# Optimization experiments

Measured on AMD Instinct MI355X. Metric: run time of the kernel, lower is better.

Reference implementation:

```python
import jax, jax.numpy as jnp
import numpy as np

ALPHA = 0.2  # leaky relu slope
NEG_BIG = -9e15


def setup_inputs() -> dict:
    key = jax.random.key(0)
    k1, k2, k3, k4 = jax.random.split(key, 4)
    B, N, Fin, Fout = 8, 2048, 128, 128
    h = jax.random.normal(k1, (B, N, Fin), dtype=jnp.float32)
    adj = jax.random.randint(k2, (N, N), 0, 2, dtype=jnp.int32)
    # xavier_uniform with gain=1.414
    limW = 1.414 * np.sqrt(6.0 / (Fin + Fout))
    W = jax.random.uniform(k3, (Fin, Fout), minval=-limW, maxval=limW, dtype=jnp.float32)
    lima = 1.414 * np.sqrt(6.0 / (2 * Fout + 1))
    a = jax.random.uniform(k4, (2 * Fout, 1), minval=-lima, maxval=lima, dtype=jnp.float32)
    return {"h": h, "adj": adj, "W": W, "a": a}


def reference(h, adj, W, a):
    # Wh: [B, N, F]
    Wh = jnp.einsum("bnf,fo->bno", h, W)
    Fout = W.shape[1]
    a1, a2 = a[:Fout, 0], a[Fout:, 0]  # [F], [F]
    # Additive score decomposition (same math as concat trick):
    # e[b,i,j] = leakyrelu(Wh_i . a1 + Wh_j . a2)
    s1 = Wh @ a1  # [B, N] (source/query part)
    s2 = Wh @ a2  # [B, N] (target part)
    e = s1[:, :, None] + s2[:, None, :]  # [B, N, N]
    e = jnp.where(e > 0, e, ALPHA * e)   # leaky relu
    e = jnp.where(adj[None, :, :] > 0, e, NEG_BIG)
    attention = jax.nn.softmax(e, axis=2)  # [B, N, N]
    # dropout is identity in eval mode
    h_prime = jnp.einsum("bij,bjf->bif", attention, Wh)
    return h_prime
```

## Files before the change

### kernel.cpp

```cpp
#include <hip/hip_runtime.h>
#include <hip/hip_bf16.h>
#include <stdint.h>

#define ALPHA 0.2f

typedef __attribute__((ext_vector_type(8))) short bf16x8;
typedef __attribute__((ext_vector_type(4))) float f32x4;

__device__ __forceinline__ short f2bf(float f) {
    union { float f; uint32_t u; } c; c.f = f;
    uint32_t u = c.u + 0x7FFF + ((c.u >> 16) & 1);
    return (short)(u >> 16);
}

__global__ __launch_bounds__(256) void pack_adj_kernel(
        const int* __restrict__ adj, uint8_t* __restrict__ bytes,
        const float* __restrict__ W, short* __restrict__ WTg) {
    int t = blockIdx.x * 256 + threadIdx.x;
    const int4* a4 = reinterpret_cast<const int4*>(adj) + (size_t)t * 2;
    int4 x0 = a4[0], x1 = a4[1];
    uint32_t m = 0;
    m |= (x0.x > 0) ? 1u   : 0u;  m |= (x0.y > 0) ? 2u   : 0u;
    m |= (x0.z > 0) ? 4u   : 0u;  m |= (x0.w > 0) ? 8u   : 0u;
    m |= (x1.x > 0) ? 16u  : 0u;  m |= (x1.y > 0) ? 32u  : 0u;
    m |= (x1.z > 0) ? 64u  : 0u;  m |= (x1.w > 0) ? 128u : 0u;
    bytes[t] = (uint8_t)m;

    if (blockIdx.x < 64) {
        int idx = blockIdx.x * 256 + threadIdx.x;
        int k = idx >> 7, f = idx & 127;
        WTg[f * 128 + k] = f2bf(W[k * 128 + f]);
    }
}

__global__ __launch_bounds__(256) void wh_kernel(
        const float* __restrict__ h, const short* __restrict__ WTg,
        const float* __restrict__ a, short* __restrict__ whT,
        float* __restrict__ s1g, float* __restrict__ s2g) {
    __shared__ float sred[4][2][16];
    __shared__ short tr[4][32][24];

    int tid = threadIdx.x, wid = tid >> 6, lane = tid & 63;
    int q = lane >> 4, n = lane & 15;
    int rb = blockIdx.x * 16;
    int row = rb + n;

    f32x4 acc[2] = {};
    #pragma unroll
    for (int kc = 0; kc < 4; ++kc) {
        const float* hp = h + (size_t)row * 128 + kc * 32 + q * 8;
        float4 h0 = reinterpret_cast<const float4*>(hp)[0];
        float4 h1 = reinterpret_cast<const float4*>(hp)[1];
        bf16x8 afrag;
        afrag[0] = f2bf(h0.x); afrag[1] = f2bf(h0.y);
        afrag[2] = f2bf(h0.z); afrag[3] = f2bf(h0.w);
        afrag[4] = f2bf(h1.x); afrag[5] = f2bf(h1.y);
        afrag[6] = f2bf(h1.z); afrag[7] = f2bf(h1.w);
        #pragma unroll
        for (int u = 0; u < 2; ++u) {
            int t = wid * 2 + u;
            bf16x8 bfrag = *reinterpret_cast<const bf16x8*>(
                WTg + (t * 16 + n) * 128 + kc * 32 + q * 8);
            acc[u] = __builtin_amdgcn_mfma_f32_16x16x32_bf16(afrag, bfrag, acc[u], 0, 0, 0);
        }
    }

    float p1[4] = {0.f, 0.f, 0.f, 0.f}, p2[4] = {0.f, 0.f, 0.f, 0.f};
    #pragma unroll
    for (int u = 0; u < 2; ++u) {
        int c = (wid * 2 + u) * 16 + n;
        float a1c = a[c], a2c = a[128 + c];
        #pragma unroll
        for (int r = 0; r < 4; ++r) {
            p1[r] += acc[u][r] * a1c;
            p2[r] += acc[u][r] * a2c;
        }
    }
    #pragma unroll
    for (int d = 1; d < 16; d <<= 1) {
        #pragma unroll
        for (int r = 0; r < 4; ++r) {
            p1[r] += __shfl_xor(p1[r], d);
            p2[r] += __shfl_xor(p2[r], d);
        }
    }
    if (n == 0) {
        #pragma unroll
        for (int r = 0; r < 4; ++r) {
            sred[wid][0][q * 4 + r] = p1[r];
            sred[wid][1][q * 4 + r] = p2[r];
        }
    }

    #pragma unroll
    for (int u = 0; u < 2; ++u)
        #pragma unroll
        for (int r = 0; r < 4; ++r)
            tr[wid][u * 16 + n][q * 4 + r] = f2bf(acc[u][r]);
    __syncthreads();

    if (wid == 0 && lane < 16) {
        float v1 = 0.f, v2 = 0.f;
        #pragma unroll
        for (int v = 0; v < 4; ++v) { v1 += sred[v][0][lane]; v2 += sred[v][1][lane]; }
        s1g[rb + lane] = v1;
        s2g[rb + lane] = v2;
    }

    int bb = rb >> 11, jr = rb & 2047;
    int fl = lane & 31, jh = lane >> 5;
    bf16x8 v = *reinterpret_cast<const bf16x8*>(&tr[wid][fl][jh * 8]);
    int f = wid * 32 + fl;
    *reinterpret_cast<bf16x8*>(whT + ((size_t)(bb * 128 + f) * 2048) + jr + jh * 8) = v;
}

__global__ __launch_bounds__(512) void attn_kernel(
        const short* __restrict__ whT, const float* __restrict__ s1g,
        const float* __restrict__ s2g, const uint8_t* __restrict__ adjb,
        float* __restrict__ out) {
    __shared__ f32x4 buf[8][8][64];
    __shared__ float lds_ds[8][2][16];

    int wid = threadIdx.x >> 6, lane = threadIdx.x & 63;
    int q = lane >> 4, n = lane & 15;
    int b  = blockIdx.x >> 6;
    int ib = (blockIdx.x & 63) * 32;
    int rowA = ib + n, rowB = ib + 16 + n;

    float s1A = s1g[b * 2048 + rowA];
    float s1B = s1g[b * 2048 + rowB];
    const float*   s2b  = s2g + b * 2048;
    const short*   whTb = whT + (size_t)b * 262144;
    const uint8_t* adjA = adjb + (size_t)rowA * 256;
    const uint8_t* adjB = adjb + (size_t)rowB * 256;

    f32x4 accA[8] = {}, accB[8] = {};
    float dsA = 0.f, dsB = 0.f;
    int jbase = wid * 256;

    for (int c = 0; c < 8; ++c) {
        int k0 = jbase + c * 32 + q * 8;
        uint32_t mA = adjA[k0 >> 3];
        uint32_t mB = adjB[k0 >> 3];
        float4 s2a = *reinterpret_cast<const float4*>(s2b + k0);
        float4 s2c = *reinterpret_cast<const float4*>(s2b + k0 + 4);
        float s2arr[8] = {s2a.x, s2a.y, s2a.z, s2a.w, s2c.x, s2c.y, s2c.z, s2c.w};

        bf16x8 afA, afB;
        #pragma unroll
        for (int j = 0; j < 8; ++j) {
            float eA = s1A + s2arr[j];
            eA = fmaxf(eA, ALPHA * eA);
            float pA = ((mA >> j) & 1) ? __expf(eA) : 0.0f;
            dsA += pA; afA[j] = f2bf(pA);
            float eB = s1B + s2arr[j];
            eB = fmaxf(eB, ALPHA * eB);
            float pB = ((mB >> j) & 1) ? __expf(eB) : 0.0f;
            dsB += pB; afB[j] = f2bf(pB);
        }

        const short* bp = whTb + k0;
        #pragma unroll
        for (int t = 0; t < 8; ++t) {
            bf16x8 bf = *reinterpret_cast<const bf16x8*>(bp + (size_t)(t * 16 + n) * 2048);
            accA[t] = __builtin_amdgcn_mfma_f32_16x16x32_bf16(afA, bf, accA[t], 0, 0, 0);
            accB[t] = __builtin_amdgcn_mfma_f32_16x16x32_bf16(afB, bf, accB[t], 0, 0, 0);
        }
    }

    dsA += __shfl_xor(dsA, 16); dsA += __shfl_xor(dsA, 32);
    dsB += __shfl_xor(dsB, 16); dsB += __shfl_xor(dsB, 32);
    if (q == 0) { lds_ds[wid][0][n] = dsA; lds_ds[wid][1][n] = dsB; }

    #pragma unroll
    for (int i = 0; i < 8; ++i) buf[wid][i][lane] = accA[i];
    __syncthreads();

    f32x4 sA = buf[0][wid][lane];
    #pragma unroll
    for (int v = 1; v < 8; ++v) sA += buf[v][wid][lane];

    float dAt = 0.f, dBt = 0.f;
    #pragma unroll
    for (int v = 0; v < 8; ++v) { dAt += lds_ds[v][0][n]; dBt += lds_ds[v][1][n]; }
    float rdA[4], rdB[4];
    #pragma unroll
    for (int r = 0; r < 4; ++r) {
        rdA[r] = 1.0f / __shfl(dAt, q * 4 + r);
        rdB[r] = 1.0f / __shfl(dBt, q * 4 + r);
    }

    size_t ob = ((size_t)b * 2048 + ib) * 128;
    #pragma unroll
    for (int r = 0; r < 4; ++r)
        out[ob + (size_t)(q * 4 + r) * 128 + wid * 16 + n] = sA[r] * rdA[r];
    __syncthreads();

    #pragma unroll
    for (int i = 0; i < 8; ++i) buf[wid][i][lane] = accB[i];
    __syncthreads();

    f32x4 sB = buf[0][wid][lane];
    #pragma unroll
    for (int v = 1; v < 8; ++v) sB += buf[v][wid][lane];
    #pragma unroll
    for (int r = 0; r < 4; ++r)
        out[ob + (size_t)(16 + q * 4 + r) * 128 + wid * 16 + n] = sB[r] * rdB[r];
}

extern "C" void kernel_launch(void* const* d_in, const int* in_sizes, int n_in,
                              void* d_out, int out_size, void* d_ws, size_t ws_size,
                              hipStream_t stream) {
    const float* h   = (const float*)d_in[0];
    const int*   adj = (const int*)d_in[1];
    const float* W   = (const float*)d_in[2];
    const float* a   = (const float*)d_in[3];
    float* out = (float*)d_out;

    char* ws = (char*)d_ws;
    short* whT = (short*)ws;
    float* s1  = (float*)(ws + 4194304);
    float* s2  = (float*)(ws + 4259840);
    uint8_t* bytes = (uint8_t*)(ws + 4325376);

    short* WTg = (short*)d_out + (4194304 - 16384);

    pack_adj_kernel<<<2048, 256, 0, stream>>>(adj, bytes, W, WTg);
    wh_kernel<<<1024, 256, 0, stream>>>(h, WTg, a, whT, s1, s2);
    attn_kernel<<<512, 512, 0, stream>>>(whT, s1, s2, bytes, out);
}
```

Measured before the change: 127.1 us.

## Software-pipeline attention loads, halve waves per block, pack bf16 with perm

The attention kernel now runs 4 waves per block instead of 8, so each wave handles 512 columns over 16 fully unrolled steps. It double-buffers the next step's whT fragments, adjacency mask words and s2 values in registers while the current step computes. Mask reads move from bytes to 32-bit words, and the float-to-bf16 conversion uses a perm-based pack with simpler rounding. The cross-wave reduction is reshaped so each wave sums two output tiles from four partials. The aim is to hide global load latency behind exp and MFMA work, at the cost of higher register pressure under a 3-blocks-per-SM launch bound and fewer waves per block.

```diff
diff --git a/kernel.cpp b/kernel.cpp
--- a/kernel.cpp
+++ b/kernel.cpp
@@ -11,6 +11,12 @@
     union { float f; uint32_t u; } c; c.f = f;
     uint32_t u = c.u + 0x7FFF + ((c.u >> 16) & 1);
     return (short)(u >> 16);
+}
+
+__device__ __forceinline__ uint32_t pk_bf16(float lo, float hi) {
+    union { float f; uint32_t u; } a, b;
+    a.f = lo; b.f = hi;
+    return __builtin_amdgcn_perm(b.u + 0x8000u, a.u + 0x8000u, 0x07060302u);
 }
 
 __global__ __launch_bounds__(256) void pack_adj_kernel(
@@ -114,57 +120,86 @@
     *reinterpret_cast<bf16x8*>(whT + ((size_t)(bb * 128 + f) * 2048) + jr + jh * 8) = v;
 }
 
-__global__ __launch_bounds__(512) void attn_kernel(
+__global__ __launch_bounds__(256, 3) void attn_kernel(
         const short* __restrict__ whT, const float* __restrict__ s1g,
         const float* __restrict__ s2g, const uint8_t* __restrict__ adjb,
         float* __restrict__ out) {
-    __shared__ f32x4 buf[8][8][64];
-    __shared__ float lds_ds[8][2][16];
+    __shared__ f32x4 buf[4][8][64];
+    __shared__ float lds_ds[4][2][16];
 
     int wid = threadIdx.x >> 6, lane = threadIdx.x & 63;
     int q = lane >> 4, n = lane & 15;
     int b  = blockIdx.x >> 6;
     int ib = (blockIdx.x & 63) * 32;
-    int rowA = ib + n, rowB = ib + 16 + n;
+    int rowA = ib + n, rowB = rowA + 16;
 
     float s1A = s1g[b * 2048 + rowA];
     float s1B = s1g[b * 2048 + rowB];
-    const float*   s2b  = s2g + b * 2048;
-    const short*   whTb = whT + (size_t)b * 262144;
-    const uint8_t* adjA = adjb + (size_t)rowA * 256;
-    const uint8_t* adjB = adjb + (size_t)rowB * 256;
+    const float* s2b = s2g + b * 2048;
+    const short* whTb = whT + (size_t)b * 262144;
+    const uint32_t* admA = reinterpret_cast<const uint32_t*>(adjb + (size_t)rowA * 256);
+    const uint32_t* admB = reinterpret_cast<const uint32_t*>(adjb + (size_t)rowB * 256);
+
+    int jbase = wid * 512;
+    const short* bpn = whTb + n * 2048 + q * 8;
 
     f32x4 accA[8] = {}, accB[8] = {};
     float dsA = 0.f, dsB = 0.f;
-    int jbase = wid * 256;
-
-    for (int c = 0; c < 8; ++c) {
-        int k0 = jbase + c * 32 + q * 8;
-        uint32_t mA = adjA[k0 >> 3];
-        uint32_t mB = adjB[k0 >> 3];
-        float4 s2a = *reinterpret_cast<const float4*>(s2b + k0);
-        float4 s2c = *reinterpret_cast<const float4*>(s2b + k0 + 4);
-        float s2arr[8] = {s2a.x, s2a.y, s2a.z, s2a.w, s2c.x, s2c.y, s2c.z, s2c.w};
-
-        bf16x8 afA, afB;
+
+    bf16x8 nb[2][8];
+    uint32_t mwA[2], mwB[2];
+    float4 s2l[2], s2h[2];
+
+    {
+        int k0 = jbase;
+        mwA[0] = admA[k0 >> 5];
+        mwB[0] = admB[k0 >> 5];
+        s2l[0] = *reinterpret_cast<const float4*>(s2b + k0 + q * 8);
+        s2h[0] = *reinterpret_cast<const float4*>(s2b + k0 + q * 8 + 4);
+        #pragma unroll
+        for (int t = 0; t < 8; ++t)
+            nb[0][t] = *reinterpret_cast<const bf16x8*>(bpn + t * 32768 + k0);
+    }
+
+    #pragma unroll
+    for (int c = 0; c < 16; ++c) {
+        const int cur = c & 1, nxt = cur ^ 1;
+        int k1 = jbase + ((c + 1) & 15) * 32;
+        mwA[nxt] = admA[k1 >> 5];
+        mwB[nxt] = admB[k1 >> 5];
+        s2l[nxt] = *reinterpret_cast<const float4*>(s2b + k1 + q * 8);
+        s2h[nxt] = *reinterpret_cast<const float4*>(s2b + k1 + q * 8 + 4);
+        #pragma unroll
+        for (int t = 0; t < 8; ++t)
+            nb[nxt][t] = *reinterpret_cast<const bf16x8*>(bpn + t * 32768 + k1);
+
+        uint32_t mA = mwA[cur] >> (q * 8);
+        uint32_t mB = mwB[cur] >> (q * 8);
+        float s2arr[8] = {s2l[cur].x, s2l[cur].y, s2l[cur].z, s2l[cur].w,
+                          s2h[cur].x, s2h[cur].y, s2h[cur].z, s2h[cur].w};
+        float pA[8], pB[8];
         #pragma unroll
         for (int j = 0; j < 8; ++j) {
             float eA = s1A + s2arr[j];
             eA = fmaxf(eA, ALPHA * eA);
-            float pA = ((mA >> j) & 1) ? __expf(eA) : 0.0f;
-            dsA += pA; afA[j] = f2bf(pA);
+            float vA = ((mA >> j) & 1) ? __expf(eA) : 0.0f;
+            dsA += vA; pA[j] = vA;
             float eB = s1B + s2arr[j];
             eB = fmaxf(eB, ALPHA * eB);
-            float pB = ((mB >> j) & 1) ? __expf(eB) : 0.0f;
-            dsB += pB; afB[j] = f2bf(pB);
-        }
-
-        const short* bp = whTb + k0;
+            float vB = ((mB >> j) & 1) ? __expf(eB) : 0.0f;
+            dsB += vB; pB[j] = vB;
+        }
+        union { uint32_t u[4]; bf16x8 v; } cvA, cvB;
+        #pragma unroll
+        for (int p = 0; p < 4; ++p) {
+            cvA.u[p] = pk_bf16(pA[2 * p], pA[2 * p + 1]);
+            cvB.u[p] = pk_bf16(pB[2 * p], pB[2 * p + 1]);
+        }
+
         #pragma unroll
         for (int t = 0; t < 8; ++t) {
-            bf16x8 bf = *reinterpret_cast<const bf16x8*>(bp + (size_t)(t * 16 + n) * 2048);
-            accA[t] = __builtin_amdgcn_mfma_f32_16x16x32_bf16(afA, bf, accA[t], 0, 0, 0);
-            accB[t] = __builtin_amdgcn_mfma_f32_16x16x32_bf16(afB, bf, accB[t], 0, 0, 0);
+            accA[t] = __builtin_amdgcn_mfma_f32_16x16x32_bf16(cvA.v, nb[cur][t], accA[t], 0, 0, 0);
+            accB[t] = __builtin_amdgcn_mfma_f32_16x16x32_bf16(cvB.v, nb[cur][t], accB[t], 0, 0, 0);
         }
     }
 
@@ -176,13 +211,12 @@
     for (int i = 0; i < 8; ++i) buf[wid][i][lane] = accA[i];
     __syncthreads();
 
-    f32x4 sA = buf[0][wid][lane];
-    #pragma unroll
-    for (int v = 1; v < 8; ++v) sA += buf[v][wid][lane];
-
-    float dAt = 0.f, dBt = 0.f;
-    #pragma unroll
-    for (int v = 0; v < 8; ++v) { dAt += lds_ds[v][0][n]; dBt += lds_ds[v][1][n]; }
+    int t0 = wid * 2, t1 = wid * 2 + 1;
+    f32x4 rA0 = buf[0][t0][lane] + buf[1][t0][lane] + buf[2][t0][lane] + buf[3][t0][lane];
+    f32x4 rA1 = buf[0][t1][lane] + buf[1][t1][lane] + buf[2][t1][lane] + buf[3][t1][lane];
+
+    float dAt = lds_ds[0][0][n] + lds_ds[1][0][n] + lds_ds[2][0][n] + lds_ds[3][0][n];
+    float dBt = lds_ds[0][1][n] + lds_ds[1][1][n] + lds_ds[2][1][n] + lds_ds[3][1][n];
     float rdA[4], rdB[4];
     #pragma unroll
     for (int r = 0; r < 4; ++r) {
@@ -192,20 +226,23 @@
 
     size_t ob = ((size_t)b * 2048 + ib) * 128;
     #pragma unroll
-    for (int r = 0; r < 4; ++r)
-        out[ob + (size_t)(q * 4 + r) * 128 + wid * 16 + n] = sA[r] * rdA[r];
+    for (int r = 0; r < 4; ++r) {
+        out[ob + (size_t)(q * 4 + r) * 128 + t0 * 16 + n] = rA0[r] * rdA[r];
+        out[ob + (size_t)(q * 4 + r) * 128 + t1 * 16 + n] = rA1[r] * rdA[r];
+    }
     __syncthreads();
 
     #pragma unroll
     for (int i = 0; i < 8; ++i) buf[wid][i][lane] = accB[i];
     __syncthreads();
 
-    f32x4 sB = buf[0][wid][lane];
-    #pragma unroll
-    for (int v = 1; v < 8; ++v) sB += buf[v][wid][lane];
-    #pragma unroll
-    for (int r = 0; r < 4; ++r)
-        out[ob + (size_t)(16 + q * 4 + r) * 128 + wid * 16 + n] = sB[r] * rdB[r];
+    f32x4 rB0 = buf[0][t0][lane] + buf[1][t0][lane] + buf[2][t0][lane] + buf[3][t0][lane];
+    f32x4 rB1 = buf[0][t1][lane] + buf[1][t1][lane] + buf[2][t1][lane] + buf[3][t1][lane];
+    #pragma unroll
+    for (int r = 0; r < 4; ++r) {
+        out[ob + (size_t)(16 + q * 4 + r) * 128 + t0 * 16 + n] = rB0[r] * rdB[r];
+        out[ob + (size_t)(16 + q * 4 + r) * 128 + t1 * 16 + n] = rB1[r] * rdB[r];
+    }
 }
 
 extern "C" void kernel_launch(void* const* d_in, const int* in_sizes, int n_in,
@@ -227,5 +264,5 @@
 
     pack_adj_kernel<<<2048, 256, 0, stream>>>(adj, bytes, W, WTg);
     wh_kernel<<<1024, 256, 0, stream>>>(h, WTg, a, whT, s1, s2);
-    attn_kernel<<<512, 512, 0, stream>>>(whT, s1, s2, bytes, out);
-}
+    attn_kernel<<<512, 256, 0, stream>>>(whT, s1, s2, bytes, out);
+}
```

After: 165.7 us. 30.4% more time.
